# Kernel optimization log

Measured on AMD Instinct MI355X. Metric: run time of the kernel, lower is better.

The kernel has to match this reference:

```python
import jax, jax.numpy as jnp
import numpy as np

K_NN = 4  # hard-coded k in get_graph_feature(x, k=4)


def _conv1(h, Wm, s, b):
    # 1x1 conv1d + folded-BN (scale/shift) + ReLU
    return jax.nn.relu(jnp.einsum('oc,bcn->bon', Wm, h) * s[:, None] + b[:, None])


def _conv2(h, Wm, s, b):
    # 1x1 conv2d + folded-BN + ReLU
    return jax.nn.relu(jnp.einsum('oc,bcnk->bonk', Wm, h) * s[:, None, None] + b[:, None, None])


def _forward(x, W_dup, s_dup, b_dup, W_c1, s_c1, b_c1,
             W2a, s2a, b2a, W2b, s2b, b2b, W2c, s2c, b2c,
             W3a, s3a, b3a, W3b, s3b, b3b, W4a, bias4a, W4b, bias4b):
    B = x.shape[0]
    h = _conv1(x, W_dup, s_dup, b_dup)           # (B,256,1024)
    h = h.reshape(B, 128, 2048)                  # duplicate points: (B,128,2048)
    h = _conv1(h, W_c1, s_c1, b_c1)              # (B,64,2048)
    g = jnp.max(h, axis=2, keepdims=True)        # max_pool1d over all 2048 -> (B,64,1)
    # knn on 64-d features: pairwise = -||xi-xj||^2, topk picks nearest (self included)
    xx = jnp.sum(h * h, axis=1, keepdims=True)   # (B,1,P)
    inner = -2.0 * jnp.einsum('bcn,bcm->bnm', h, h)
    pd = -xx - inner - jnp.swapaxes(xx, 1, 2)    # (B,P,P)
    idx = jax.lax.top_k(pd, K_NN)[1]             # (B,P,k)
    xt = jnp.swapaxes(h, 1, 2)                   # (B,P,C)
    nb = xt[jnp.arange(B)[:, None, None], idx]   # gather neighbors: (B,P,k,C)
    ctr = xt[:, :, None, :]
    feat = jnp.concatenate([nb - ctr, jnp.broadcast_to(ctr, nb.shape)], axis=-1)  # (B,P,k,2C)
    feat = jnp.transpose(feat, (0, 3, 1, 2))     # (B,128,P,k)
    feat = _conv2(feat, W2a, s2a, b2a)
    feat = _conv2(feat, W2b, s2b, b2b)
    feat = _conv2(feat, W2c, s2c, b2c)           # (B,64,P,k)
    local = jnp.max(feat, axis=3)                # max over k -> (B,64,P)
    g = _conv1(g, W3a, s3a, b3a)
    g = _conv1(g, W3b, s3b, b3b)                 # (B,128,1)
    final = jnp.concatenate([local, jnp.broadcast_to(g, (B, 128, local.shape[2]))], axis=1)  # (B,192,P)
    h4 = jax.nn.relu(jnp.einsum('oc,bcn->bon', W4a, final) + bias4a[:, None])  # (B,256,P)
    out = jnp.einsum('oc,bcn->bon', W4b, h4) + bias4b[:, None]                 # (B,3,P)
    return out


def setup_inputs() -> dict:
    key = jax.random.key(0)
    ks = list(jax.random.split(key, 30))
    W = lambda k, o, c: jax.random.normal(k, (o, c), jnp.float32) * 0.05
    sc = lambda k, c: 1.0 + 0.1 * jax.random.normal(k, (c,), jnp.float32)
    bs = lambda k, c: 0.1 * jax.random.normal(k, (c,), jnp.float32)
    return {
        'search_keypoint': jax.random.normal(ks[0], (8, 128, 1024), jnp.float32),
        'W_dup': W(ks[1], 256, 128), 's_dup': sc(ks[2], 256), 'b_dup': bs(ks[3], 256),
        'W_c1': W(ks[4], 64, 128), 's_c1': sc(ks[5], 64), 'b_c1': bs(ks[6], 64),
        'W2a': W(ks[7], 64, 128), 's2a': sc(ks[8], 64), 'b2a': bs(ks[9], 64),
        'W2b': W(ks[10], 64, 64), 's2b': sc(ks[11], 64), 'b2b': bs(ks[12], 64),
        'W2c': W(ks[13], 64, 64), 's2c': sc(ks[14], 64), 'b2c': bs(ks[15], 64),
        'W3a': W(ks[16], 128, 64), 's3a': sc(ks[17], 128), 'b3a': bs(ks[18], 128),
        'W3b': W(ks[19], 128, 128), 's3b': sc(ks[20], 128), 'b3b': bs(ks[21], 128),
        'W4a': W(ks[22], 256, 192), 'bias4a': bs(ks[23], 256),
        'W4b': W(ks[24], 3, 256), 'bias4b': bs(ks[25], 3),
    }


def reference(search_keypoint, W_dup, s_dup, b_dup, W_c1, s_c1, b_c1,
              W2a, s2a, b2a, W2b, s2b, b2b, W2c, s2c, b2c,
              W3a, s3a, b3a, W3b, s3b, b3b, W4a, bias4a, W4b, bias4b):
    return _forward(search_keypoint, W_dup, s_dup, b_dup, W_c1, s_c1, b_c1,
                    W2a, s2a, b2a, W2b, s2b, b2b, W2c, s2c, b2c,
                    W3a, s3a, b3a, W3b, s3b, b3b, W4a, bias4a, W4b, bias4b)
```

## Files before the change

### kernel.cpp

```cpp
#include <hip/hip_runtime.h>
#include <float.h>

typedef __attribute__((ext_vector_type(8))) short short8;
typedef __attribute__((ext_vector_type(4))) float f32x4;
typedef unsigned short u16;
typedef unsigned long long u64;

static constexpr size_t OFF_W     = 0;
static constexpr size_t OFF_YZ    = 131072;
static constexpr size_t OFF_Zf    = 1179648;
static constexpr size_t OFF_FEATR = 2228224;
static constexpr size_t OFF_FIN   = 6422528;
static constexpr size_t OFF_XX    = 9568256;
static constexpr size_t OFF_G     = 9584640;
static constexpr size_t OFF_G3BS  = 9592832;
static constexpr size_t WS_FLOATS = 9659392;

static constexpr size_t WO_DUP = 0;
static constexpr size_t WO_C1  = 32768;
static constexpr size_t WO_2A  = 40960;
static constexpr size_t WO_2B  = 49152;
static constexpr size_t WO_2C  = 53248;
static constexpr size_t WO_4A  = 57344;

__device__ __forceinline__ void gl_lds16(const void* g, void* l) {
    __builtin_amdgcn_global_load_lds(
        (const __attribute__((address_space(1))) void*)g,
        (__attribute__((address_space(3))) void*)l, 16, 0, 0);
}

__device__ __forceinline__ u16 f2bf(float x) {
    union { float f; unsigned int u; } v; v.f = x;
    unsigned int r = v.u + 0x7fffu + ((v.u >> 16) & 1u);
    return (u16)(r >> 16);
}
__device__ __forceinline__ float bf2f(u16 h) {
    union { unsigned int u; float f; } v; v.u = ((unsigned int)h) << 16;
    return v.f;
}
__device__ __forceinline__ void split2(float x, u16& h, u16& l) {
    h = f2bf(x);
    l = f2bf(x - bf2f(h));
}

__device__ __forceinline__ unsigned int fmap(float f) {
    unsigned int u = __float_as_uint(f);
    return u ^ ((unsigned int)((int)u >> 31) | 0x80000000u);
}
__device__ __forceinline__ u64 mkkey(float f, int m) {
    return ((u64)fmap(f) << 32) | (unsigned int)(2047 - m);
}
static __device__ __forceinline__ void ins4k(u64 k, u64 bk[4])
{
#pragma unroll
    for (int s = 0; s < 4; ++s) {
        bool better = k > bk[s];
        u64 t = bk[s];
        bk[s] = better ? k : bk[s];
        k = better ? t : k;
    }
}

__global__ __launch_bounds__(256) void wsplit(
    const float* W_dup, const float* W_c1, const float* W2a,
    const float* W2b, const float* W2c, const float* W4a,
    u16* whi, u16* wlo)
{
    int t = blockIdx.x * 256 + threadIdx.x;
    float v;
    if      (t < 40960) v = (t < 32768) ? W_dup[t] : W_c1[t - 32768];
    else if (t < 53248) v = (t < 49152) ? W2a[t - 40960] : W2b[t - 49152];
    else                v = (t < 57344) ? W2c[t - 53248] : W4a[t - 57344];
    u16 h, l; split2(v, h, l);
    whi[t] = h; wlo[t] = l;
}

__global__ __launch_bounds__(256) void tsplit_x(const float* x, u16* xthi, u16* xtlo)
{
    const int b = blockIdx.z, c0 = blockIdx.y * 64, n0 = blockIdx.x * 64;
    const int t = threadIdx.x;
    __shared__ float tile[64][65];
    const float* xb = x + ((size_t)b * 128 + c0) * 1024;
#pragma unroll
    for (int i = 0; i < 16; ++i) {
        int c = i * 4 + (t >> 6), n = t & 63;
        tile[c][n] = xb[(size_t)c * 1024 + n0 + n];
    }
    __syncthreads();
#pragma unroll
    for (int i = 0; i < 16; ++i) {
        int n = i * 4 + (t >> 6), c = t & 63;
        u16 h, l; split2(tile[c][n], h, l);
        const size_t o = ((size_t)b * 1024 + n0 + n) * 128 + c0 + c;
        xthi[o] = h; xtlo[o] = l;
    }
}

template<int K, int NT, int OMODE, bool RELU, bool XX = false>
__global__ __launch_bounds__(256) void conv_mf(
    const u16* __restrict__ Whi, const u16* __restrict__ Wlo, int wstride,
    const float* __restrict__ scale, const float* __restrict__ bias,
    const u16* Ahi, const u16* Alo,
    u16* ohi, u16* olo, float* of, float* of2, int Ns,
    const float* __restrict__ W2, const float* __restrict__ bias2, float* xxout)
{
    constexpr int KS = K / 32;
    const int t = threadIdx.x;
    const int wu = t >> 6;
    const int lane = t & 63;
    const int j = lane & 15, q = lane >> 4;
    const int n0g = blockIdx.x * 64 + wu * 16;

    short8 a_hi[KS], a_lo[KS];
    const u16* arow_h = Ahi + (size_t)(n0g + j) * K + q * 8;
    const u16* arow_l = Alo + (size_t)(n0g + j) * K + q * 8;
#pragma unroll
    for (int ks = 0; ks < KS; ++ks) {
        a_hi[ks] = *(const short8*)(arow_h + ks * 32);
        a_lo[ks] = *(const short8*)(arow_l + ks * 32);
    }

    const int wofs = (OMODE == 4) ? (int)(blockIdx.y * 64) : 0;
    const int obase = (OMODE == 4 || OMODE == 5) ? 0 : blockIdx.y * NT;
    float sq[4] = {0.f, 0.f, 0.f, 0.f};
    float p[3][4];
    if constexpr (OMODE == 5) {
#pragma unroll
        for (int oo = 0; oo < 3; ++oo)
#pragma unroll
            for (int r = 0; r < 4; ++r) p[oo][r] = 0.f;
    }

#pragma unroll
    for (int ct = 0; ct < NT; ++ct) {
        const int o = (obase + ct) * 16 + j;
        const u16* wr_h = Whi + (size_t)o * wstride + wofs + q * 8;
        const u16* wr_l = Wlo + (size_t)o * wstride + wofs + q * 8;
        f32x4 acc = (f32x4){0.f, 0.f, 0.f, 0.f};
#pragma unroll
        for (int ks = 0; ks < KS; ++ks) {
            short8 bh = *(const short8*)(wr_h + ks * 32);
            short8 bl = *(const short8*)(wr_l + ks * 32);
            acc = __builtin_amdgcn_mfma_f32_16x16x32_bf16(a_hi[ks], bh, acc, 0, 0, 0);
            acc = __builtin_amdgcn_mfma_f32_16x16x32_bf16(a_hi[ks], bl, acc, 0, 0, 0);
            acc = __builtin_amdgcn_mfma_f32_16x16x32_bf16(a_lo[ks], bh, acc, 0, 0, 0);
        }
        const float sc = scale ? scale[o] : 1.0f;
        const float bi = bias ? bias[o] : 0.0f;
        float v[4];
#pragma unroll
        for (int r = 0; r < 4; ++r) {
            v[r] = acc[r] * sc + bi;
            if (RELU) v[r] = fmaxf(v[r], 0.f);
            if (XX) sq[r] += v[r] * v[r];
        }
        if constexpr (OMODE == 0) {
#pragma unroll
            for (int r = 0; r < 4; ++r) {
                u16 h, l; split2(v[r], h, l);
                const size_t row = n0g + q * 4 + r;
                ohi[row * Ns + o] = h; olo[row * Ns + o] = l;
            }
        } else if constexpr (OMODE == 3) {
            const int b = n0g >> 10;
            const int nn = (n0g & 1023) + q * 4;
            const size_t rowbase = ((size_t)b << 11) + nn + ((o & 1) << 10);
            const int col = o >> 1;
#pragma unroll
            for (int r = 0; r < 4; ++r) {
                u16 h, l; split2(v[r], h, l);
                ohi[(rowbase + r) * 128 + col] = h;
                olo[(rowbase + r) * 128 + col] = l;
            }
        } else if constexpr (OMODE == 4) {
            float* dst = blockIdx.y ? of2 : of;
#pragma unroll
            for (int r = 0; r < 4; ++r)
                dst[(size_t)(n0g + q * 4 + r) * Ns + o] = v[r];
        } else if constexpr (OMODE == 5) {
            float w0 = W2[o], w1 = W2[256 + o], w2 = W2[512 + o];
#pragma unroll
            for (int r = 0; r < 4; ++r) {
                p[0][r] += w0 * v[r];
                p[1][r] += w1 * v[r];
                p[2][r] += w2 * v[r];
            }
        }
    }

    if constexpr (XX) {
#pragma unroll
        for (int r = 0; r < 4; ++r) {
#pragma unroll
            for (int mask = 1; mask < 16; mask <<= 1)
                sq[r] += __shfl_xor(sq[r], mask, 64);
        }
        if (j == 0) {
#pragma unroll
            for (int r = 0; r < 4; ++r)
                xxout[n0g + q * 4 + r] = sq[r];
        }
    }
    if constexpr (OMODE == 5) {
#pragma unroll
        for (int oo = 0; oo < 3; ++oo)
#pragma unroll
            for (int r = 0; r < 4; ++r) {
#pragma unroll
                for (int mask = 1; mask < 16; mask <<= 1)
                    p[oo][r] += __shfl_xor(p[oo][r], mask, 64);
            }
        if (j == 0) {
            const int row0 = n0g + q * 4;
            const int b = row0 >> 11;
#pragma unroll
            for (int r = 0; r < 4; ++r) {
                const int n = (row0 + r) & 2047;
#pragma unroll
                for (int oo = 0; oo < 3; ++oo)
                    of[((size_t)b * 3 + oo) * 2048 + n] = p[oo][r] + bias2[oo];
            }
        }
    }
}

struct __align__(16) KBuf {
    u16 hi[4096];
    u16 lo[4096];
    float xm[64];
};

__global__ __launch_bounds__(256) void knn_topk(const u16* __restrict__ thi,
                                                const u16* __restrict__ tlo,
                                                const float* __restrict__ xx,
                                                u64* __restrict__ part)
{
    const int b    = blockIdx.z;
    const int mh   = blockIdx.y;
    const int t    = threadIdx.x;
    const int wu   = __builtin_amdgcn_readfirstlane(t >> 6);
    const int lane = t & 63;
    const int j    = lane & 15;
    const int q    = lane >> 4;
    const int nrow0 = blockIdx.x * 64 + wu * 16;

    const u16* th = thi + (size_t)b * 2048 * 64;
    const u16* tl = tlo + (size_t)b * 2048 * 64;
    const float* xb = xx + (size_t)b * 2048;

    __shared__ KBuf sb[2];

    const size_t arow = (size_t)(nrow0 + j) * 64;
    short8 ah0 = *(const short8*)(th + arow + q * 8);
    short8 ah1 = *(const short8*)(th + arow + 32 + q * 8);
    short8 al0 = *(const short8*)(tl + arow + q * 8);
    short8 al1 = *(const short8*)(tl + arow + 32 + q * 8);

    u64 bk[4][4];
#pragma unroll
    for (int r = 0; r < 4; ++r)
#pragma unroll
        for (int s = 0; s < 4; ++s) bk[r][s] = 0ull;

    const int mbeg = mh * 1024;

#define KNN_STAGE(BUF, M0)                                                        \
    {                                                                             \
        const u16* sh = th + (size_t)((M0) + lane) * 64;                          \
        const u16* sl = tl + (size_t)((M0) + lane) * 64;                          \
        gl_lds16(sh + (2 * wu) * 8,     &sb[BUF].hi[(2 * wu) * 512]);             \
        gl_lds16(sh + (2 * wu + 1) * 8, &sb[BUF].hi[(2 * wu + 1) * 512]);         \
        gl_lds16(sl + (2 * wu) * 8,     &sb[BUF].lo[(2 * wu) * 512]);             \
        gl_lds16(sl + (2 * wu + 1) * 8, &sb[BUF].lo[(2 * wu + 1) * 512]);         \
        if (wu == 0 && lane < 16) gl_lds16(xb + (M0) + lane * 4, &sb[BUF].xm[0]); \
    }

    KNN_STAGE(0, mbeg)

    for (int tt = 0; tt < 16; ++tt) {
        __syncthreads();
        if (tt < 15) KNN_STAGE((tt + 1) & 1, mbeg + (tt + 1) * 64)
        const KBuf& bf = sb[tt & 1];
        const int m0 = mbeg + tt * 64;

        float pds[4][4];
#pragma unroll
        for (int sub = 0; sub < 4; ++sub) {
            const int ml = sub * 16 + j;
            short8 bh0 = *(const short8*)&bf.hi[(q) * 512 + ml * 8];
            short8 bh1 = *(const short8*)&bf.hi[(4 + q) * 512 + ml * 8];
            short8 bl0 = *(const short8*)&bf.lo[(q) * 512 + ml * 8];
            short8 bl1 = *(const short8*)&bf.lo[(4 + q) * 512 + ml * 8];
            const float xmv = bf.xm[ml];
            f32x4 accA = (f32x4){0.f, 0.f, 0.f, 0.f};
            f32x4 accB = (f32x4){0.f, 0.f, 0.f, 0.f};
            accA = __builtin_amdgcn_mfma_f32_16x16x32_bf16(ah0, bh0, accA, 0, 0, 0);
            accB = __builtin_amdgcn_mfma_f32_16x16x32_bf16(ah1, bh1, accB, 0, 0, 0);
            accA = __builtin_amdgcn_mfma_f32_16x16x32_bf16(ah0, bl0, accA, 0, 0, 0);
            accB = __builtin_amdgcn_mfma_f32_16x16x32_bf16(ah1, bl1, accB, 0, 0, 0);
            accA = __builtin_amdgcn_mfma_f32_16x16x32_bf16(al0, bh0, accA, 0, 0, 0);
            accB = __builtin_amdgcn_mfma_f32_16x16x32_bf16(al1, bh1, accB, 0, 0, 0);
            accA = __builtin_amdgcn_mfma_f32_16x16x32_bf16(al0, bl0, accA, 0, 0, 0);
            accB = __builtin_amdgcn_mfma_f32_16x16x32_bf16(al1, bl1, accB, 0, 0, 0);
#pragma unroll
            for (int r = 0; r < 4; ++r)
                pds[sub][r] = __builtin_fmaf(2.f, accA[r] + accB[r], -xmv);
        }

#pragma unroll
        for (int r = 0; r < 4; ++r) {
            float mx = fmaxf(fmaxf(pds[0][r], pds[1][r]), fmaxf(pds[2][r], pds[3][r]));
            if (fmap(mx) >= (unsigned int)(bk[r][3] >> 32)) {
#pragma unroll
                for (int sub = 0; sub < 4; ++sub) {
                    u64 key = mkkey(pds[sub][r], m0 + sub * 16 + j);
                    if (key > bk[r][3]) ins4k(key, bk[r]);
                }
            }
        }
    }
#undef KNN_STAGE

#pragma unroll
    for (int rr = 0; rr < 4; ++rr) {
#pragma unroll
        for (int mask = 1; mask < 16; mask <<= 1) {
            u64 pk[4];
#pragma unroll
            for (int s = 0; s < 4; ++s) pk[s] = __shfl_xor(bk[rr][s], mask, 64);
#pragma unroll
            for (int s = 0; s < 4; ++s) ins4k(pk[s], bk[rr]);
        }
    }
    if (j == 0) {
#pragma unroll
        for (int r = 0; r < 4; ++r) {
            const int nrow = nrow0 + q * 4 + r;
            u64* pp = part + (((size_t)b * 2 + mh) * 2048 + nrow) * 4;
            pp[0] = bk[r][0]; pp[1] = bk[r][1]; pp[2] = bk[r][2]; pp[3] = bk[r][3];
        }
    }
}

__global__ __launch_bounds__(256) void gmaxp(const u16* __restrict__ h2thi,
                                             const u16* __restrict__ h2tlo,
                                             float* __restrict__ gp)
{
    const int bs = blockIdx.x;
    const int b = bs >> 4, slice = bs & 15;
    const int c = threadIdx.x & 63, rg = threadIdx.x >> 6;
    float m = -FLT_MAX;
    const size_t base = (size_t)b * 2048 + slice * 128 + rg * 32;
    for (int i = 0; i < 32; ++i) {
        const size_t n = base + i;
        m = fmaxf(m, bf2f(h2thi[n * 64 + c]) + bf2f(h2tlo[n * 64 + c]));
    }
    __shared__ float red[4][64];
    red[rg][c] = m;
    __syncthreads();
    if (threadIdx.x < 64)
        gp[(size_t)bs * 64 + threadIdx.x] =
            fmaxf(fmaxf(red[0][threadIdx.x], red[1][threadIdx.x]),
                  fmaxf(red[2][threadIdx.x], red[3][threadIdx.x]));
}

__global__ __launch_bounds__(128) void gconv_kernel(
    const float* __restrict__ gp,
    const float* __restrict__ W3a, const float* __restrict__ s3a, const float* __restrict__ b3a,
    const float* __restrict__ W3b, const float* __restrict__ s3b, const float* __restrict__ b3b,
    u16* __restrict__ g3bh, u16* __restrict__ g3bl)
{
    const int b = blockIdx.x;
    const int t = threadIdx.x;
    __shared__ float gl[64], ga[128];
    if (t < 64) {
        float m = -FLT_MAX;
#pragma unroll
        for (int s = 0; s < 16; ++s)
            m = fmaxf(m, gp[((size_t)b * 16 + s) * 64 + t]);
        gl[t] = m;
    }
    __syncthreads();
    float a = 0.f;
#pragma unroll
    for (int c = 0; c < 64; ++c) a += W3a[t * 64 + c] * gl[c];
    ga[t] = fmaxf(a * s3a[t] + b3a[t], 0.f);
    __syncthreads();
    float o = 0.f;
#pragma unroll
    for (int c = 0; c < 128; ++c) o += W3b[t * 128 + c] * ga[c];
    float v = fmaxf(o * s3b[t] + b3b[t], 0.f);
    u16 h, l; split2(v, h, l);
    g3bh[(size_t)b * 128 + t] = h;
    g3bl[(size_t)b * 128 + t] = l;
}

__global__ __launch_bounds__(256) void fused_edge(
    const u64* __restrict__ part,
    const float* __restrict__ y, const float* __restrict__ z,
    const float* __restrict__ s2a, const float* __restrict__ b2a,
    const u16* __restrict__ w2bh, const u16* __restrict__ w2bl,
    const float* __restrict__ s2b, const float* __restrict__ b2b,
    const u16* __restrict__ w2ch, const u16* __restrict__ w2cl,
    const float* __restrict__ s2c, const float* __restrict__ b2c,
    const u16* __restrict__ g3bh, const u16* __restrict__ g3bl,
    u16* __restrict__ finhi, u16* __restrict__ finlo)
{
    const int t = threadIdx.x;
    const int wu = t >> 6;
    const int lane = t & 63;
    const int j = lane & 15, q = lane >> 4;
    const int gb = blockIdx.x;
    const int b = gb >> 7;
    const int n0 = (gb & 127) * 16;

    __shared__ u16 plh[64 * 72];
    __shared__ u16 pll[64 * 72];
    __shared__ int sidx[64];

    if (lane < 4) {
        const int n = n0 + wu * 4 + lane;
        u64 fk[4] = {0ull, 0ull, 0ull, 0ull};
        const u64* p0 = part + (((size_t)b * 2 + 0) * 2048 + n) * 4;
        const u64* p1 = part + (((size_t)b * 2 + 1) * 2048 + n) * 4;
#pragma unroll
        for (int s = 0; s < 4; ++s) ins4k(p0[s], fk);
#pragma unroll
        for (int s = 0; s < 4; ++s) ins4k(p1[s], fk);
        int4 ii;
        ii.x = 2047 - (int)(fk[0] & 0x7ff);
        ii.y = 2047 - (int)(fk[1] & 0x7ff);
        ii.z = 2047 - (int)(fk[2] & 0x7ff);
        ii.w = 2047 - (int)(fk[3] & 0x7ff);
        *(int4*)&sidx[wu * 16 + lane * 4] = ii;
    }

    {
        const int row = lane >> 2;
        const int c0 = (lane & 3) * 16;
        const int id = sidx[wu * 16 + row];
        const int nfull = n0 + wu * 4 + (row >> 2);
        const float* yb = y + (size_t)b * 2048 * 64;
        const float* yi = yb + (size_t)id * 64;
        const float* yn = yb + (size_t)nfull * 64;
        const float* zn = z + ((size_t)b * 2048 + nfull) * 64;
        u16* oh = &plh[(wu * 16 + row) * 72 + c0];
        u16* ol = &pll[(wu * 16 + row) * 72 + c0];
#pragma unroll
        for (int cc = 0; cc < 16; cc += 4) {
            const int c = c0 + cc;
            float4 a  = *(const float4*)(yi + c);
            float4 bq = *(const float4*)(yn + c);
            float4 cq = *(const float4*)(zn + c);
            float4 sv = *(const float4*)(s2a + c);
            float4 bb = *(const float4*)(b2a + c);
            float v0 = fmaxf((a.x - bq.x + cq.x) * sv.x + bb.x, 0.f);
            float v1 = fmaxf((a.y - bq.y + cq.y) * sv.y + bb.y, 0.f);
            float v2 = fmaxf((a.z - bq.z + cq.z) * sv.z + bb.z, 0.f);
            float v3 = fmaxf((a.w - bq.w + cq.w) * sv.w + bb.w, 0.f);
            union { u16 u[4]; uint2 v; } ph, pl;
            split2(v0, ph.u[0], pl.u[0]);
            split2(v1, ph.u[1], pl.u[1]);
            split2(v2, ph.u[2], pl.u[2]);
            split2(v3, ph.u[3], pl.u[3]);
            *(uint2*)(oh + cc) = ph.v;
            *(uint2*)(ol + cc) = pl.v;
        }
    }

    {
        const int abase = (wu * 16 + j) * 72 + q * 8;
        short8 ah0 = *(const short8*)&plh[abase];
        short8 ah1 = *(const short8*)&plh[abase + 32];
        short8 al0 = *(const short8*)&pll[abase];
        short8 al1 = *(const short8*)&pll[abase + 32];
#pragma unroll
        for (int ct = 0; ct < 4; ++ct) {
            const int o = ct * 16 + j;
            short8 bh0 = *(const short8*)(w2bh + (size_t)o * 64 + q * 8);
            short8 bh1 = *(const short8*)(w2bh + (size_t)o * 64 + 32 + q * 8);
            short8 bl0 = *(const short8*)(w2bl + (size_t)o * 64 + q * 8);
            short8 bl1 = *(const short8*)(w2bl + (size_t)o * 64 + 32 + q * 8);
            f32x4 acc = (f32x4){0.f, 0.f, 0.f, 0.f};
            acc = __builtin_amdgcn_mfma_f32_16x16x32_bf16(ah0, bh0, acc, 0, 0, 0);
            acc = __builtin_amdgcn_mfma_f32_16x16x32_bf16(ah0, bl0, acc, 0, 0, 0);
            acc = __builtin_amdgcn_mfma_f32_16x16x32_bf16(al0, bh0, acc, 0, 0, 0);
            acc = __builtin_amdgcn_mfma_f32_16x16x32_bf16(ah1, bh1, acc, 0, 0, 0);
            acc = __builtin_amdgcn_mfma_f32_16x16x32_bf16(ah1, bl1, acc, 0, 0, 0);
            acc = __builtin_amdgcn_mfma_f32_16x16x32_bf16(al1, bh1, acc, 0, 0, 0);
            const float sc = s2b[o], bi = b2b[o];
#pragma unroll
            for (int r = 0; r < 4; ++r) {
                float v = fmaxf(acc[r] * sc + bi, 0.f);
                u16 h, l; split2(v, h, l);
                const int row = wu * 16 + q * 4 + r;
                plh[row * 72 + o] = h;
                pll[row * 72 + o] = l;
            }
        }
    }

    {
        const int abase = (wu * 16 + j) * 72 + q * 8;
        short8 ah0 = *(const short8*)&plh[abase];
        short8 ah1 = *(const short8*)&plh[abase + 32];
        short8 al0 = *(const short8*)&pll[abase];
        short8 al1 = *(const short8*)&pll[abase + 32];
        const size_t finrow = (size_t)b * 2048 + n0 + wu * 4 + q;
#pragma unroll
        for (int ct = 0; ct < 4; ++ct) {
            const int o = ct * 16 + j;
            short8 bh0 = *(const short8*)(w2ch + (size_t)o * 64 + q * 8);
            short8 bh1 = *(const short8*)(w2ch + (size_t)o * 64 + 32 + q * 8);
            short8 bl0 = *(const short8*)(w2cl + (size_t)o * 64 + q * 8);
            short8 bl1 = *(const short8*)(w2cl + (size_t)o * 64 + 32 + q * 8);
            f32x4 acc = (f32x4){0.f, 0.f, 0.f, 0.f};
            acc = __builtin_amdgcn_mfma_f32_16x16x32_bf16(ah0, bh0, acc, 0, 0, 0);
            acc = __builtin_amdgcn_mfma_f32_16x16x32_bf16(ah0, bl0, acc, 0, 0, 0);
            acc = __builtin_amdgcn_mfma_f32_16x16x32_bf16(al0, bh0, acc, 0, 0, 0);
            acc = __builtin_amdgcn_mfma_f32_16x16x32_bf16(ah1, bh1, acc, 0, 0, 0);
            acc = __builtin_amdgcn_mfma_f32_16x16x32_bf16(ah1, bl1, acc, 0, 0, 0);
            acc = __builtin_amdgcn_mfma_f32_16x16x32_bf16(al1, bh1, acc, 0, 0, 0);
            const float sc = s2c[o], bi = b2c[o];
            float m = -FLT_MAX;
#pragma unroll
            for (int r = 0; r < 4; ++r)
                m = fmaxf(m, fmaxf(acc[r] * sc + bi, 0.f));
            u16 h, l; split2(m, h, l);
            finhi[finrow * 192 + o] = h;
            finlo[finrow * 192 + o] = l;
        }

        const int r = lane >> 4;
        const int chunk = lane & 15;
        const size_t br = (size_t)b * 2048 + n0 + wu * 4 + r;
        short8 gh = *(const short8*)(g3bh + (size_t)b * 128 + chunk * 8);
        short8 gl = *(const short8*)(g3bl + (size_t)b * 128 + chunk * 8);
        *(short8*)(finhi + br * 192 + 64 + chunk * 8) = gh;
        *(short8*)(finlo + br * 192 + 64 + chunk * 8) = gl;
    }
}

extern "C" void kernel_launch(void* const* d_in, const int* in_sizes, int n_in,
                              void* d_out, int out_size, void* d_ws, size_t ws_size,
                              hipStream_t stream)
{
    const float* x     = (const float*)d_in[0];
    const float* W_dup = (const float*)d_in[1];
    const float* s_dup = (const float*)d_in[2];
    const float* b_dup = (const float*)d_in[3];
    const float* W_c1  = (const float*)d_in[4];
    const float* s_c1  = (const float*)d_in[5];
    const float* b_c1  = (const float*)d_in[6];
    const float* W2a   = (const float*)d_in[7];
    const float* s2a   = (const float*)d_in[8];
    const float* b2a   = (const float*)d_in[9];
    const float* W2b   = (const float*)d_in[10];
    const float* s2b   = (const float*)d_in[11];
    const float* b2b   = (const float*)d_in[12];
    const float* W2c   = (const float*)d_in[13];
    const float* s2c   = (const float*)d_in[14];
    const float* b2c   = (const float*)d_in[15];
    const float* W3a   = (const float*)d_in[16];
    const float* s3a   = (const float*)d_in[17];
    const float* b3a   = (const float*)d_in[18];
    const float* W3b   = (const float*)d_in[19];
    const float* s3b   = (const float*)d_in[20];
    const float* b3b   = (const float*)d_in[21];
    const float* W4a   = (const float*)d_in[22];
    const float* b4a   = (const float*)d_in[23];
    const float* W4b   = (const float*)d_in[24];
    const float* b4b   = (const float*)d_in[25];

    if (ws_size < WS_FLOATS * sizeof(float)) return;

    float* ws = (float*)d_ws;
    u16* whi   = (u16*)(ws + OFF_W);
    u16* wlo   = whi + 131072;
    u16* xthi  = (u16*)(ws + OFF_FEATR);
    u16* xtlo  = xthi + 1048576;
    u16* h1rhi = (u16*)(ws + OFF_YZ);
    u16* h1rlo = h1rhi + 2097152;
    u16* h2thi = (u16*)(ws + OFF_FIN);
    u16* h2tlo = h2thi + 1048576;
    u64* part  = (u64*)(ws + OFF_FEATR);
    float* y    = ws + OFF_YZ;
    float* z    = ws + OFF_Zf;
    u16* finhi  = (u16*)(ws + OFF_FIN);
    u16* finlo  = finhi + 3145728;
    float* xxb  = ws + OFF_XX;
    float* gp   = ws + OFF_G;
    u16* g3bh   = (u16*)(ws + OFF_G3BS);
    u16* g3bl   = g3bh + 1024;
    float* out  = (float*)d_out;

    wsplit<<<416, 256, 0, stream>>>(W_dup, W_c1, W2a, W2b, W2c, W4a, whi, wlo);
    tsplit_x<<<dim3(16, 2, 8), 256, 0, stream>>>(x, xthi, xtlo);
    conv_mf<128, 4, 3, true><<<dim3(128, 4), 256, 0, stream>>>(
        whi + WO_DUP, wlo + WO_DUP, 128, s_dup, b_dup, xthi, xtlo,
        h1rhi, h1rlo, nullptr, nullptr, 128, nullptr, nullptr, nullptr);
    conv_mf<128, 4, 0, true, true><<<dim3(256, 1), 256, 0, stream>>>(
        whi + WO_C1, wlo + WO_C1, 128, s_c1, b_c1, h1rhi, h1rlo,
        h2thi, h2tlo, nullptr, nullptr, 64, nullptr, nullptr, xxb);
    gmaxp<<<128, 256, 0, stream>>>(h2thi, h2tlo, gp);
    knn_topk<<<dim3(32, 2, 8), 256, 0, stream>>>(h2thi, h2tlo, xxb, part);
    conv_mf<64, 4, 4, false><<<dim3(256, 2), 256, 0, stream>>>(
        whi + WO_2A, wlo + WO_2A, 128, nullptr, nullptr, h2thi, h2tlo,
        nullptr, nullptr, y, z, 64, nullptr, nullptr, nullptr);
    gconv_kernel<<<8, 128, 0, stream>>>(gp, W3a, s3a, b3a, W3b, s3b, b3b, g3bh, g3bl);
    fused_edge<<<1024, 256, 0, stream>>>(
        part, y, z, s2a, b2a,
        whi + WO_2B, wlo + WO_2B, s2b, b2b,
        whi + WO_2C, wlo + WO_2C, s2c, b2c,
        g3bh, g3bl, finhi, finlo);
    conv_mf<192, 16, 5, true><<<dim3(256, 1), 256, 0, stream>>>(
        whi + WO_4A, wlo + WO_4A, 192, nullptr, b4a, finhi, finlo,
        nullptr, nullptr, out, nullptr, 256, W4b, b4b, nullptr);
}
```

Baseline: 263.7 us.

## Fuse conv_dup, conv_c1, global max and conv2a into one backbone kernel; split knn wider

Replaces the separate conv_dup, conv_c1, gmaxp and conv2a launches with one backbone kernel per 16-point tile. It keeps the intermediate h1 and h2 activations in LDS instead of writing them to global memory, and computes per-tile channel maxima and squared norms in place. The knn search is split into four column quarters instead of two to expose more blocks, and fused_edge merges four partial top-k lists. This removes global round trips and launches, at the cost of a small grid (512 blocks) and redundant weight loads per block.

```diff
diff --git a/kernel.cpp b/kernel.cpp
--- a/kernel.cpp
+++ b/kernel.cpp
@@ -13,8 +13,8 @@
 static constexpr size_t OFF_FIN   = 6422528;
 static constexpr size_t OFF_XX    = 9568256;
 static constexpr size_t OFF_G     = 9584640;
-static constexpr size_t OFF_G3BS  = 9592832;
-static constexpr size_t WS_FLOATS = 9659392;
+static constexpr size_t OFF_G3BS  = 9617408;
+static constexpr size_t WS_FLOATS = 9652736;
 
 static constexpr size_t WO_DUP = 0;
 static constexpr size_t WO_C1  = 32768;
@@ -96,99 +96,106 @@
     }
 }
 
-template<int K, int NT, int OMODE, bool RELU, bool XX = false>
-__global__ __launch_bounds__(256) void conv_mf(
-    const u16* __restrict__ Whi, const u16* __restrict__ Wlo, int wstride,
-    const float* __restrict__ scale, const float* __restrict__ bias,
-    const u16* Ahi, const u16* Alo,
-    u16* ohi, u16* olo, float* of, float* of2, int Ns,
-    const float* __restrict__ W2, const float* __restrict__ bias2, float* xxout)
-{
-    constexpr int KS = K / 32;
+__global__ __launch_bounds__(256) void backbone(
+    const u16* __restrict__ xthi, const u16* __restrict__ xtlo,
+    const u16* __restrict__ whi, const u16* __restrict__ wlo,
+    const float* __restrict__ s_dup, const float* __restrict__ b_dup,
+    const float* __restrict__ s_c1, const float* __restrict__ b_c1,
+    u16* __restrict__ h2thi, u16* __restrict__ h2tlo,
+    float* __restrict__ xxb, float* __restrict__ gp,
+    float* __restrict__ y, float* __restrict__ z)
+{
     const int t = threadIdx.x;
     const int wu = t >> 6;
     const int lane = t & 63;
     const int j = lane & 15, q = lane >> 4;
-    const int n0g = blockIdx.x * 64 + wu * 16;
-
-    short8 a_hi[KS], a_lo[KS];
-    const u16* arow_h = Ahi + (size_t)(n0g + j) * K + q * 8;
-    const u16* arow_l = Alo + (size_t)(n0g + j) * K + q * 8;
-#pragma unroll
-    for (int ks = 0; ks < KS; ++ks) {
-        a_hi[ks] = *(const short8*)(arow_h + ks * 32);
-        a_lo[ks] = *(const short8*)(arow_l + ks * 32);
-    }
-
-    const int wofs = (OMODE == 4) ? (int)(blockIdx.y * 64) : 0;
-    const int obase = (OMODE == 4 || OMODE == 5) ? 0 : blockIdx.y * NT;
-    float sq[4] = {0.f, 0.f, 0.f, 0.f};
-    float p[3][4];
-    if constexpr (OMODE == 5) {
-#pragma unroll
-        for (int oo = 0; oo < 3; ++oo)
-#pragma unroll
-            for (int r = 0; r < 4; ++r) p[oo][r] = 0.f;
-    }
-
-#pragma unroll
-    for (int ct = 0; ct < NT; ++ct) {
-        const int o = (obase + ct) * 16 + j;
-        const u16* wr_h = Whi + (size_t)o * wstride + wofs + q * 8;
-        const u16* wr_l = Wlo + (size_t)o * wstride + wofs + q * 8;
-        f32x4 acc = (f32x4){0.f, 0.f, 0.f, 0.f};
-#pragma unroll
-        for (int ks = 0; ks < KS; ++ks) {
-            short8 bh = *(const short8*)(wr_h + ks * 32);
-            short8 bl = *(const short8*)(wr_l + ks * 32);
-            acc = __builtin_amdgcn_mfma_f32_16x16x32_bf16(a_hi[ks], bh, acc, 0, 0, 0);
-            acc = __builtin_amdgcn_mfma_f32_16x16x32_bf16(a_hi[ks], bl, acc, 0, 0, 0);
-            acc = __builtin_amdgcn_mfma_f32_16x16x32_bf16(a_lo[ks], bh, acc, 0, 0, 0);
-        }
-        const float sc = scale ? scale[o] : 1.0f;
-        const float bi = bias ? bias[o] : 0.0f;
-        float v[4];
-#pragma unroll
-        for (int r = 0; r < 4; ++r) {
-            v[r] = acc[r] * sc + bi;
-            if (RELU) v[r] = fmaxf(v[r], 0.f);
-            if (XX) sq[r] += v[r] * v[r];
-        }
-        if constexpr (OMODE == 0) {
+    const int nb = blockIdx.x;
+    const int b  = blockIdx.y;
+    const int n0 = nb * 16;
+
+    __shared__ __align__(16) u16 h1h[32 * 136], h1l[32 * 136];
+    __shared__ __align__(16) u16 h2h[32 * 72],  h2l[32 * 72];
+    __shared__ float xxp[2][2][16];
+    __shared__ float gpart[2][64];
+
+    {
+        const size_t arow = ((size_t)b * 1024 + n0 + j) * 128;
+        short8 ahv[4], alv[4];
+#pragma unroll
+        for (int ks = 0; ks < 4; ++ks) {
+            ahv[ks] = *(const short8*)(xthi + arow + q * 8 + ks * 32);
+            alv[ks] = *(const short8*)(xtlo + arow + q * 8 + ks * 32);
+        }
+        const u16* wdh = whi + WO_DUP;
+        const u16* wdl = wlo + WO_DUP;
+#pragma unroll
+        for (int ci = 0; ci < 4; ++ci) {
+            const int o = (wu * 4 + ci) * 16 + j;
+            f32x4 acc = (f32x4){0.f, 0.f, 0.f, 0.f};
+#pragma unroll
+            for (int ks = 0; ks < 4; ++ks) {
+                short8 bh = *(const short8*)(wdh + (size_t)o * 128 + q * 8 + ks * 32);
+                short8 bl = *(const short8*)(wdl + (size_t)o * 128 + q * 8 + ks * 32);
+                acc = __builtin_amdgcn_mfma_f32_16x16x32_bf16(ahv[ks], bh, acc, 0, 0, 0);
+                acc = __builtin_amdgcn_mfma_f32_16x16x32_bf16(ahv[ks], bl, acc, 0, 0, 0);
+                acc = __builtin_amdgcn_mfma_f32_16x16x32_bf16(alv[ks], bh, acc, 0, 0, 0);
+            }
+            const float sc = s_dup[o], bi = b_dup[o];
+            const int lrbase = (j & 1) * 16;
+            const int col = (wu * 4 + ci) * 8 + (j >> 1);
 #pragma unroll
             for (int r = 0; r < 4; ++r) {
-                u16 h, l; split2(v[r], h, l);
-                const size_t row = n0g + q * 4 + r;
-                ohi[row * Ns + o] = h; olo[row * Ns + o] = l;
-            }
-        } else if constexpr (OMODE == 3) {
-            const int b = n0g >> 10;
-            const int nn = (n0g & 1023) + q * 4;
-            const size_t rowbase = ((size_t)b << 11) + nn + ((o & 1) << 10);
-            const int col = o >> 1;
+                float v = fmaxf(acc[r] * sc + bi, 0.f);
+                u16 h, l; split2(v, h, l);
+                const int lr = lrbase + q * 4 + r;
+                h1h[lr * 136 + col] = h;
+                h1l[lr * 136 + col] = l;
+            }
+        }
+    }
+    __syncthreads();
+
+    {
+        const int g = wu >> 1, ch = wu & 1;
+        short8 ahv[4], alv[4];
+#pragma unroll
+        for (int ks = 0; ks < 4; ++ks) {
+            ahv[ks] = *(const short8*)&h1h[(g * 16 + j) * 136 + q * 8 + ks * 32];
+            alv[ks] = *(const short8*)&h1l[(g * 16 + j) * 136 + q * 8 + ks * 32];
+        }
+        const u16* wch = whi + WO_C1;
+        const u16* wcl = wlo + WO_C1;
+        float sq[4] = {0.f, 0.f, 0.f, 0.f};
+        float cm[2];
+#pragma unroll
+        for (int ci = 0; ci < 2; ++ci) {
+            const int o = (ch * 2 + ci) * 16 + j;
+            f32x4 acc = (f32x4){0.f, 0.f, 0.f, 0.f};
+#pragma unroll
+            for (int ks = 0; ks < 4; ++ks) {
+                short8 bh = *(const short8*)(wch + (size_t)o * 128 + q * 8 + ks * 32);
+                short8 bl = *(const short8*)(wcl + (size_t)o * 128 + q * 8 + ks * 32);
+                acc = __builtin_amdgcn_mfma_f32_16x16x32_bf16(ahv[ks], bh, acc, 0, 0, 0);
+                acc = __builtin_amdgcn_mfma_f32_16x16x32_bf16(ahv[ks], bl, acc, 0, 0, 0);
+                acc = __builtin_amdgcn_mfma_f32_16x16x32_bf16(alv[ks], bh, acc, 0, 0, 0);
+            }
+            const float sc = s_c1[o], bi = b_c1[o];
+            float vmax = -FLT_MAX;
 #pragma unroll
             for (int r = 0; r < 4; ++r) {
-                u16 h, l; split2(v[r], h, l);
-                ohi[(rowbase + r) * 128 + col] = h;
-                olo[(rowbase + r) * 128 + col] = l;
-            }
-        } else if constexpr (OMODE == 4) {
-            float* dst = blockIdx.y ? of2 : of;
-#pragma unroll
-            for (int r = 0; r < 4; ++r)
-                dst[(size_t)(n0g + q * 4 + r) * Ns + o] = v[r];
-        } else if constexpr (OMODE == 5) {
-            float w0 = W2[o], w1 = W2[256 + o], w2 = W2[512 + o];
-#pragma unroll
-            for (int r = 0; r < 4; ++r) {
-                p[0][r] += w0 * v[r];
-                p[1][r] += w1 * v[r];
-                p[2][r] += w2 * v[r];
-            }
-        }
-    }
-
-    if constexpr (XX) {
+                float v = fmaxf(acc[r] * sc + bi, 0.f);
+                sq[r] += v * v;
+                vmax = fmaxf(vmax, v);
+                u16 h, l; split2(v, h, l);
+                const size_t R = (size_t)b * 2048 + g * 1024 + n0 + q * 4 + r;
+                h2thi[R * 64 + o] = h;
+                h2tlo[R * 64 + o] = l;
+                const int lr = g * 16 + q * 4 + r;
+                h2h[lr * 72 + o] = h;
+                h2l[lr * 72 + o] = l;
+            }
+            cm[ci] = vmax;
+        }
 #pragma unroll
         for (int r = 0; r < 4; ++r) {
 #pragma unroll
@@ -197,28 +204,57 @@
         }
         if (j == 0) {
 #pragma unroll
-            for (int r = 0; r < 4; ++r)
-                xxout[n0g + q * 4 + r] = sq[r];
-        }
-    }
-    if constexpr (OMODE == 5) {
-#pragma unroll
-        for (int oo = 0; oo < 3; ++oo)
+            for (int r = 0; r < 4; ++r) xxp[g][ch][q * 4 + r] = sq[r];
+        }
+#pragma unroll
+        for (int ci = 0; ci < 2; ++ci) {
+            cm[ci] = fmaxf(cm[ci], __shfl_xor(cm[ci], 16, 64));
+            cm[ci] = fmaxf(cm[ci], __shfl_xor(cm[ci], 32, 64));
+        }
+        if (q == 0) {
+#pragma unroll
+            for (int ci = 0; ci < 2; ++ci)
+                gpart[g][(ch * 2 + ci) * 16 + j] = cm[ci];
+        }
+    }
+    __syncthreads();
+
+    if (t < 32) {
+        const int g = t >> 4, i = t & 15;
+        xxb[(size_t)b * 2048 + g * 1024 + n0 + i] = xxp[g][0][i] + xxp[g][1][i];
+    }
+    if (t >= 64 && t < 128) {
+        const int c = t - 64;
+        gp[((size_t)b * 64 + nb) * 64 + c] = fmaxf(gpart[0][c], gpart[1][c]);
+    }
+
+    {
+        const int g = wu & 1, half = wu >> 1;
+        short8 ahv[2], alv[2];
+#pragma unroll
+        for (int ks = 0; ks < 2; ++ks) {
+            ahv[ks] = *(const short8*)&h2h[(g * 16 + j) * 72 + q * 8 + ks * 32];
+            alv[ks] = *(const short8*)&h2l[(g * 16 + j) * 72 + q * 8 + ks * 32];
+        }
+        const u16* w2h = whi + WO_2A;
+        const u16* w2l = wlo + WO_2A;
+        float* dst = half ? z : y;
+#pragma unroll
+        for (int ci = 0; ci < 4; ++ci) {
+            const int o = ci * 16 + j;
+            f32x4 acc = (f32x4){0.f, 0.f, 0.f, 0.f};
+#pragma unroll
+            for (int ks = 0; ks < 2; ++ks) {
+                short8 bh = *(const short8*)(w2h + (size_t)o * 128 + half * 64 + q * 8 + ks * 32);
+                short8 bl = *(const short8*)(w2l + (size_t)o * 128 + half * 64 + q * 8 + ks * 32);
+                acc = __builtin_amdgcn_mfma_f32_16x16x32_bf16(ahv[ks], bh, acc, 0, 0, 0);
+                acc = __builtin_amdgcn_mfma_f32_16x16x32_bf16(ahv[ks], bl, acc, 0, 0, 0);
+                acc = __builtin_amdgcn_mfma_f32_16x16x32_bf16(alv[ks], bh, acc, 0, 0, 0);
+            }
 #pragma unroll
             for (int r = 0; r < 4; ++r) {
-#pragma unroll
-                for (int mask = 1; mask < 16; mask <<= 1)
-                    p[oo][r] += __shfl_xor(p[oo][r], mask, 64);
-            }
-        if (j == 0) {
-            const int row0 = n0g + q * 4;
-            const int b = row0 >> 11;
-#pragma unroll
-            for (int r = 0; r < 4; ++r) {
-                const int n = (row0 + r) & 2047;
-#pragma unroll
-                for (int oo = 0; oo < 3; ++oo)
-                    of[((size_t)b * 3 + oo) * 2048 + n] = p[oo][r] + bias2[oo];
+                const size_t R = (size_t)b * 2048 + g * 1024 + n0 + q * 4 + r;
+                dst[R * 64 + o] = acc[r];
             }
         }
     }
@@ -236,7 +272,7 @@
                                                 u64* __restrict__ part)
 {
     const int b    = blockIdx.z;
-    const int mh   = blockIdx.y;
+    const int mq   = blockIdx.y;
     const int t    = threadIdx.x;
     const int wu   = __builtin_amdgcn_readfirstlane(t >> 6);
     const int lane = t & 63;
@@ -262,7 +298,7 @@
 #pragma unroll
         for (int s = 0; s < 4; ++s) bk[r][s] = 0ull;
 
-    const int mbeg = mh * 1024;
+    const int mbeg = mq * 512;
 
 #define KNN_STAGE(BUF, M0)                                                        \
     {                                                                             \
@@ -277,9 +313,9 @@
 
     KNN_STAGE(0, mbeg)
 
-    for (int tt = 0; tt < 16; ++tt) {
+    for (int tt = 0; tt < 8; ++tt) {
         __syncthreads();
-        if (tt < 15) KNN_STAGE((tt + 1) & 1, mbeg + (tt + 1) * 64)
+        if (tt < 7) KNN_STAGE((tt + 1) & 1, mbeg + (tt + 1) * 64)
         const KBuf& bf = sb[tt & 1];
         const int m0 = mbeg + tt * 64;
 
@@ -336,32 +372,10 @@
 #pragma unroll
         for (int r = 0; r < 4; ++r) {
             const int nrow = nrow0 + q * 4 + r;
-            u64* pp = part + (((size_t)b * 2 + mh) * 2048 + nrow) * 4;
+            u64* pp = part + (((size_t)b * 4 + mq) * 2048 + nrow) * 4;
             pp[0] = bk[r][0]; pp[1] = bk[r][1]; pp[2] = bk[r][2]; pp[3] = bk[r][3];
         }
     }
-}
-
-__global__ __launch_bounds__(256) void gmaxp(const u16* __restrict__ h2thi,
-                                             const u16* __restrict__ h2tlo,
-                                             float* __restrict__ gp)
-{
-    const int bs = blockIdx.x;
-    const int b = bs >> 4, slice = bs & 15;
-    const int c = threadIdx.x & 63, rg = threadIdx.x >> 6;
-    float m = -FLT_MAX;
-    const size_t base = (size_t)b * 2048 + slice * 128 + rg * 32;
-    for (int i = 0; i < 32; ++i) {
-        const size_t n = base + i;
-        m = fmaxf(m, bf2f(h2thi[n * 64 + c]) + bf2f(h2tlo[n * 64 + c]));
-    }
-    __shared__ float red[4][64];
-    red[rg][c] = m;
-    __syncthreads();
-    if (threadIdx.x < 64)
-        gp[(size_t)bs * 64 + threadIdx.x] =
-            fmaxf(fmaxf(red[0][threadIdx.x], red[1][threadIdx.x]),
-                  fmaxf(red[2][threadIdx.x], red[3][threadIdx.x]));
 }
 
 __global__ __launch_bounds__(128) void gconv_kernel(
@@ -375,9 +389,8 @@
     __shared__ float gl[64], ga[128];
     if (t < 64) {
         float m = -FLT_MAX;
-#pragma unroll
-        for (int s = 0; s < 16; ++s)
-            m = fmaxf(m, gp[((size_t)b * 16 + s) * 64 + t]);
+        for (int s = 0; s < 64; ++s)
+            m = fmaxf(m, gp[((size_t)b * 64 + s) * 64 + t]);
         gl[t] = m;
     }
     __syncthreads();
@@ -414,19 +427,19 @@
     const int b = gb >> 7;
     const int n0 = (gb & 127) * 16;
 
-    __shared__ u16 plh[64 * 72];
-    __shared__ u16 pll[64 * 72];
+    __shared__ __align__(16) u16 plh[64 * 72];
+    __shared__ __align__(16) u16 pll[64 * 72];
     __shared__ int sidx[64];
 
     if (lane < 4) {
         const int n = n0 + wu * 4 + lane;
         u64 fk[4] = {0ull, 0ull, 0ull, 0ull};
-        const u64* p0 = part + (((size_t)b * 2 + 0) * 2048 + n) * 4;
-        const u64* p1 = part + (((size_t)b * 2 + 1) * 2048 + n) * 4;
-#pragma unroll
-        for (int s = 0; s < 4; ++s) ins4k(p0[s], fk);
-#pragma unroll
-        for (int s = 0; s < 4; ++s) ins4k(p1[s], fk);
+#pragma unroll
+        for (int qt = 0; qt < 4; ++qt) {
+            const u64* pp = part + (((size_t)b * 4 + qt) * 2048 + n) * 4;
+#pragma unroll
+            for (int s = 0; s < 4; ++s) ins4k(pp[s], fk);
+        }
         int4 ii;
         ii.x = 2047 - (int)(fk[0] & 0x7ff);
         ii.y = 2047 - (int)(fk[1] & 0x7ff);
@@ -535,9 +548,83 @@
         const int chunk = lane & 15;
         const size_t br = (size_t)b * 2048 + n0 + wu * 4 + r;
         short8 gh = *(const short8*)(g3bh + (size_t)b * 128 + chunk * 8);
-        short8 gl = *(const short8*)(g3bl + (size_t)b * 128 + chunk * 8);
+        short8 glv = *(const short8*)(g3bl + (size_t)b * 128 + chunk * 8);
         *(short8*)(finhi + br * 192 + 64 + chunk * 8) = gh;
-        *(short8*)(finlo + br * 192 + 64 + chunk * 8) = gl;
+        *(short8*)(finlo + br * 192 + 64 + chunk * 8) = glv;
+    }
+}
+
+__global__ __launch_bounds__(256) void conv_final(
+    const u16* __restrict__ Whi, const u16* __restrict__ Wlo,
+    const float* __restrict__ bias,
+    const u16* __restrict__ Ahi, const u16* __restrict__ Alo,
+    const float* __restrict__ W2, const float* __restrict__ bias2,
+    float* __restrict__ out)
+{
+    const int t = threadIdx.x;
+    const int wu = t >> 6;
+    const int lane = t & 63;
+    const int j = lane & 15, q = lane >> 4;
+    const int n0g = blockIdx.x * 64 + wu * 16;
+
+    short8 a_hi[6], a_lo[6];
+    const u16* arow_h = Ahi + (size_t)(n0g + j) * 192 + q * 8;
+    const u16* arow_l = Alo + (size_t)(n0g + j) * 192 + q * 8;
+#pragma unroll
+    for (int ks = 0; ks < 6; ++ks) {
+        a_hi[ks] = *(const short8*)(arow_h + ks * 32);
+        a_lo[ks] = *(const short8*)(arow_l + ks * 32);
+    }
+
+    float p[3][4];
+#pragma unroll
+    for (int oo = 0; oo < 3; ++oo)
+#pragma unroll
+        for (int r = 0; r < 4; ++r) p[oo][r] = 0.f;
+
+#pragma unroll
+    for (int ct = 0; ct < 16; ++ct) {
+        const int o = ct * 16 + j;
+        const u16* wr_h = Whi + (size_t)o * 192 + q * 8;
+        const u16* wr_l = Wlo + (size_t)o * 192 + q * 8;
+        f32x4 acc = (f32x4){0.f, 0.f, 0.f, 0.f};
+#pragma unroll
+        for (int ks = 0; ks < 6; ++ks) {
+            short8 bh = *(const short8*)(wr_h + ks * 32);
+            short8 bl = *(const short8*)(wr_l + ks * 32);
+            acc = __builtin_amdgcn_mfma_f32_16x16x32_bf16(a_hi[ks], bh, acc, 0, 0, 0);
+            acc = __builtin_amdgcn_mfma_f32_16x16x32_bf16(a_hi[ks], bl, acc, 0, 0, 0);
+            acc = __builtin_amdgcn_mfma_f32_16x16x32_bf16(a_lo[ks], bh, acc, 0, 0, 0);
+        }
+        const float bi = bias[o];
+        float w0 = W2[o], w1 = W2[256 + o], w2 = W2[512 + o];
+#pragma unroll
+        for (int r = 0; r < 4; ++r) {
+            float v = fmaxf(acc[r] + bi, 0.f);
+            p[0][r] += w0 * v;
+            p[1][r] += w1 * v;
+            p[2][r] += w2 * v;
+        }
+    }
+
+#pragma unroll
+    for (int oo = 0; oo < 3; ++oo)
+#pragma unroll
+        for (int r = 0; r < 4; ++r) {
+#pragma unroll
+            for (int mask = 1; mask < 16; mask <<= 1)
+                p[oo][r] += __shfl_xor(p[oo][r], mask, 64);
+        }
+    if (j == 0) {
+        const int row0 = n0g + q * 4;
+        const int b = row0 >> 11;
+#pragma unroll
+        for (int r = 0; r < 4; ++r) {
+            const int n = (row0 + r) & 2047;
+#pragma unroll
+            for (int oo = 0; oo < 3; ++oo)
+                out[((size_t)b * 3 + oo) * 2048 + n] = p[oo][r] + bias2[oo];
+        }
     }
 }
 
@@ -579,13 +666,11 @@
     u16* wlo   = whi + 131072;
     u16* xthi  = (u16*)(ws + OFF_FEATR);
     u16* xtlo  = xthi + 1048576;
-    u16* h1rhi = (u16*)(ws + OFF_YZ);
-    u16* h1rlo = h1rhi + 2097152;
-    u16* h2thi = (u16*)(ws + OFF_FIN);
-    u16* h2tlo = h2thi + 1048576;
     u64* part  = (u64*)(ws + OFF_FEATR);
     float* y    = ws + OFF_YZ;
     float* z    = ws + OFF_Zf;
+    u16* h2thi = (u16*)(ws + OFF_FIN);
+    u16* h2tlo = h2thi + 1048576;
     u16* finhi  = (u16*)(ws + OFF_FIN);
     u16* finlo  = finhi + 3145728;
     float* xxb  = ws + OFF_XX;
@@ -596,24 +681,16 @@
 
     wsplit<<<416, 256, 0, stream>>>(W_dup, W_c1, W2a, W2b, W2c, W4a, whi, wlo);
     tsplit_x<<<dim3(16, 2, 8), 256, 0, stream>>>(x, xthi, xtlo);
-    conv_mf<128, 4, 3, true><<<dim3(128, 4), 256, 0, stream>>>(
-        whi + WO_DUP, wlo + WO_DUP, 128, s_dup, b_dup, xthi, xtlo,
-        h1rhi, h1rlo, nullptr, nullptr, 128, nullptr, nullptr, nullptr);
-    conv_mf<128, 4, 0, true, true><<<dim3(256, 1), 256, 0, stream>>>(
-        whi + WO_C1, wlo + WO_C1, 128, s_c1, b_c1, h1rhi, h1rlo,
-        h2thi, h2tlo, nullptr, nullptr, 64, nullptr, nullptr, xxb);
-    gmaxp<<<128, 256, 0, stream>>>(h2thi, h2tlo, gp);
-    knn_topk<<<dim3(32, 2, 8), 256, 0, stream>>>(h2thi, h2tlo, xxb, part);
-    conv_mf<64, 4, 4, false><<<dim3(256, 2), 256, 0, stream>>>(
-        whi + WO_2A, wlo + WO_2A, 128, nullptr, nullptr, h2thi, h2tlo,
-        nullptr, nullptr, y, z, 64, nullptr, nullptr, nullptr);
+    backbone<<<dim3(64, 8), 256, 0, stream>>>(
+        xthi, xtlo, whi, wlo, s_dup, b_dup, s_c1, b_c1,
+        h2thi, h2tlo, xxb, gp, y, z);
     gconv_kernel<<<8, 128, 0, stream>>>(gp, W3a, s3a, b3a, W3b, s3b, b3b, g3bh, g3bl);
+    knn_topk<<<dim3(32, 4, 8), 256, 0, stream>>>(h2thi, h2tlo, xxb, part);
     fused_edge<<<1024, 256, 0, stream>>>(
         part, y, z, s2a, b2a,
         whi + WO_2B, wlo + WO_2B, s2b, b2b,
         whi + WO_2C, wlo + WO_2C, s2c, b2c,
         g3bh, g3bl, finhi, finlo);
-    conv_mf<192, 16, 5, true><<<dim3(256, 1), 256, 0, stream>>>(
-        whi + WO_4A, wlo + WO_4A, 192, nullptr, b4a, finhi, finlo,
-        nullptr, nullptr, out, nullptr, 256, W4b, b4b, nullptr);
-}
+    conv_final<<<256, 256, 0, stream>>>(
+        whi + WO_4A, wlo + WO_4A, b4a, finhi, finlo, W4b, b4b, out);
+}
```

Measured after the change: 268.0 us. About the same (+1.6%).
